# Performance work log

Hardware: AMD Instinct MI355X
Metric: run time of the kernel (lower is better)

## Reference

```python
import jax, jax.numpy as jnp
import numpy as np


def setup_inputs() -> dict:
    key = jax.random.key(0)
    ks = jax.random.split(key, 8)
    B, M, C, H, W = 2, 16, 256, 64, 64
    T = 1024  # transformer_dim
    return {
        "transformer_output": jax.random.normal(ks[0], (B, T), dtype=jnp.float32),
        "residual_maps": jax.random.normal(ks[1], (B, M, C, H, W), dtype=jnp.float32),
        "Wq": jax.random.normal(ks[2], (C, T), dtype=jnp.float32) * 0.02,
        "bq": jnp.zeros((C,), dtype=jnp.float32),
        "Wk": jax.random.normal(ks[3], (C, C), dtype=jnp.float32) * 0.02,
        "bk": jnp.zeros((C,), dtype=jnp.float32),
        "Wv": jax.random.normal(ks[4], (C, C), dtype=jnp.float32) * 0.02,
        "bv": jnp.zeros((C,), dtype=jnp.float32),
    }


def reference(transformer_output, residual_maps, Wq, bq, Wk, bk, Wv, bv):
    # residual_maps: [B, M, C, H, W]; single query per batch element.
    B, M, C, H, W = residual_maps.shape
    scale = C ** (-0.5)
    # Linear query projection: [B, C]
    q = transformer_output @ Wq.T + bq
    # 1x1 conv == per-pixel channel matmul: [B, M, C, H, W]
    keys = jnp.einsum("oc,bmchw->bmohw", Wk, residual_maps) + bk[None, None, :, None, None]
    values = jnp.einsum("oc,bmchw->bmohw", Wv, residual_maps) + bv[None, None, :, None, None]
    # Single-query dot-product scores per (map, pixel): [B, M, H, W]
    scores = jnp.einsum("bc,bmchw->bmhw", q, keys) * scale
    # Temporal softmax over num_maps at each spatial position
    probs = jax.nn.softmax(scores, axis=1)
    # Softmax-weighted sum of value maps: [B, C, H, W]
    out = jnp.einsum("bmhw,bmchw->bchw", probs, values)
    return out
```

## Files before the change

kernel.cpp:

```cpp
#include <hip/hip_runtime.h>

#define SCALE 0.0625f
#define ROW 36

typedef __attribute__((ext_vector_type(4))) float f32x4;
typedef __attribute__((ext_vector_type(8))) short s16x8;

__device__ __forceinline__ unsigned short f2bf(float x) {
    unsigned u = __float_as_uint(x);
    u = u + 0x7FFF + ((u >> 16) & 1);
    return (unsigned short)(u >> 16);
}

__global__ __launch_bounds__(256) void prep1_kernel(
    const float* __restrict__ TO,
    const float* __restrict__ Wq,
    const float* __restrict__ bq,
    const float* __restrict__ Wv,
    float* __restrict__ qbuf,
    unsigned short* __restrict__ WvB)
{
    const int blk = blockIdx.x;
    const int t   = threadIdx.x;
    if (blk < 16) {
        const int b    = blk >> 3;
        const int rblk = blk & 7;
        const int wv = t >> 6, l = t & 63;
        const float4* Wq4 = (const float4*)Wq;
        const float4* TO4 = (const float4*)TO;
        for (int rr = 0; rr < 8; ++rr) {
            const int c = rblk * 32 + wv * 8 + rr;
            float acc = 0.f;
#pragma unroll
            for (int i = 0; i < 4; ++i) {
                float4 wq = Wq4[c * 256 + i * 64 + l];
                float4 tv = TO4[b * 256 + i * 64 + l];
                acc = fmaf(wq.x, tv.x, acc);
                acc = fmaf(wq.y, tv.y, acc);
                acc = fmaf(wq.z, tv.z, acc);
                acc = fmaf(wq.w, tv.w, acc);
            }
#pragma unroll
            for (int mask = 1; mask < 64; mask <<= 1)
                acc += __shfl_xor(acc, mask, 64);
            if (l == 0) qbuf[b * 256 + c] = acc + bq[c];
        }
    } else {
        const int idx = blk - 16;
#pragma unroll
        for (int i = 0; i < 4; ++i) {
            const int e = idx * 4096 + i * 1024 + t * 4;
            const float4 f = ((const float4*)Wv)[e >> 2];
            ushort4 o;
            o.x = f2bf(f.x); o.y = f2bf(f.y);
            o.z = f2bf(f.z); o.w = f2bf(f.w);
            *(ushort4*)(WvB + e) = o;
        }
    }
}

__global__ __launch_bounds__(256) void prep2_kernel(
    const float* __restrict__ qbuf,
    const float* __restrict__ Wk,
    float* __restrict__ qks)
{
    const int blk = blockIdx.x;
    const int t   = threadIdx.x;
    const int b = blk >> 3, j = blk & 7;
    const int col = t & 31, chunk = t >> 5;
    const int cp = j * 32 + col;
    float partial = 0.f;
#pragma unroll 8
    for (int cc = 0; cc < 32; ++cc) {
        const int c = chunk * 32 + cc;
        partial = fmaf(qbuf[b * 256 + c], Wk[c * 256 + cp], partial);
    }
    __shared__ float r2[8][32];
    r2[chunk][col] = partial;
    __syncthreads();
    if (t < 32) {
        float s = 0.f;
#pragma unroll
        for (int k = 0; k < 8; ++k) s += r2[k][t];
        qks[b * 256 + j * 32 + t] = SCALE * s;
    }
}

__global__ __launch_bounds__(512, 2) void main_kernel(
    const float* __restrict__ X,
    const float* __restrict__ qks,
    const unsigned short* __restrict__ WvB,
    const float* __restrict__ bv,
    float* __restrict__ out)
{
    const int t    = threadIdx.x;
    const int lane = t & 63;
    const int w    = t >> 6;
    const int blk  = blockIdx.x;
    const int b    = blk >> 7;
    const int hw0  = (blk & 127) << 5;

    __shared__ float lds[2 * 256 * ROW];
    float* const buf0 = lds;
    float* const buf1 = lds + 256 * ROW;

    const int sc   = t >> 3;
    const int spxq = t & 7;
    const float4* X4 = (const float4*)X;
    const int gstage = b * 16 * 262144 + (hw0 >> 2) + spxq;

    float qk[4];
#pragma unroll
    for (int c4 = 0; c4 < 4; ++c4)
        qk[c4] = qks[b * 256 + lane + 64 * c4];

    float4 wx[4];
#pragma unroll
    for (int c4 = 0; c4 < 4; ++c4) wx[c4] = make_float4(0.f, 0.f, 0.f, 0.f);
    float lsx = 0.f, lsy = 0.f, lsz = 0.f, lsw = 0.f;

    float4 sreg[4];
#pragma unroll
    for (int r = 0; r < 4; ++r)
        sreg[r] = X4[gstage + 0 * 262144 + (sc + r * 64) * 1024];
#pragma unroll
    for (int r = 0; r < 4; ++r)
        *(float4*)&buf0[(sc + r * 64) * ROW + spxq * 4] = sreg[r];

#pragma unroll 2
    for (int m = 0; m < 16; ++m) {
        __syncthreads();
        float* const cur  = (m & 1) ? buf1 : buf0;
        float* const nxtb = (m & 1) ? buf0 : buf1;

        if (m < 15) {
#pragma unroll
            for (int r = 0; r < 4; ++r)
                sreg[r] = X4[gstage + (m + 1) * 262144 + (sc + r * 64) * 1024];
        }

        float4 v[4];
#pragma unroll
        for (int c4 = 0; c4 < 4; ++c4)
            v[c4] = *(const float4*)&cur[(lane + 64 * c4) * ROW + w * 4];

        float sx = 0.f, sy = 0.f, sz = 0.f, sw = 0.f;
#pragma unroll
        for (int c4 = 0; c4 < 4; ++c4) {
            sx = fmaf(qk[c4], v[c4].x, sx);
            sy = fmaf(qk[c4], v[c4].y, sy);
            sz = fmaf(qk[c4], v[c4].z, sz);
            sw = fmaf(qk[c4], v[c4].w, sw);
        }
#pragma unroll
        for (int mask = 1; mask < 64; mask <<= 1) {
            sx += __shfl_xor(sx, mask, 64);
            sy += __shfl_xor(sy, mask, 64);
            sz += __shfl_xor(sz, mask, 64);
            sw += __shfl_xor(sw, mask, 64);
        }
        const float e0 = __expf(sx), e1 = __expf(sy);
        const float e2 = __expf(sz), e3 = __expf(sw);
        lsx += e0; lsy += e1; lsz += e2; lsw += e3;
#pragma unroll
        for (int c4 = 0; c4 < 4; ++c4) {
            wx[c4].x = fmaf(e0, v[c4].x, wx[c4].x);
            wx[c4].y = fmaf(e1, v[c4].y, wx[c4].y);
            wx[c4].z = fmaf(e2, v[c4].z, wx[c4].z);
            wx[c4].w = fmaf(e3, v[c4].w, wx[c4].w);
        }

        if (m < 15) {
#pragma unroll
            for (int r = 0; r < 4; ++r)
                *(float4*)&nxtb[(sc + r * 64) * ROW + spxq * 4] = sreg[r];
        }
    }

    const float i0 = 1.0f / lsx, i1 = 1.0f / lsy;
    const float i2 = 1.0f / lsz, i3 = 1.0f / lsw;
#pragma unroll
    for (int c4 = 0; c4 < 4; ++c4) {
        float4 r;
        r.x = wx[c4].x * i0; r.y = wx[c4].y * i1;
        r.z = wx[c4].z * i2; r.w = wx[c4].w * i3;
        *(float4*)&buf0[(lane + 64 * c4) * ROW + w * 4] = r;
    }
    __syncthreads();

    const int px16 = lane & 15;
    const int quad = lane >> 4;

    f32x4 acc[2][2];
#pragma unroll
    for (int tl = 0; tl < 2; ++tl)
#pragma unroll
        for (int pxh = 0; pxh < 2; ++pxh)
#pragma unroll
            for (int r = 0; r < 4; ++r)
                acc[tl][pxh][r] = bv[16 * (w * 2 + tl) + quad * 4 + r];

#pragma unroll
    for (int ks = 0; ks < 8; ++ks) {
        s16x8 bfr[2];
#pragma unroll
        for (int pxh = 0; pxh < 2; ++pxh)
#pragma unroll
            for (int j = 0; j < 8; ++j)
                bfr[pxh][j] = (short)f2bf(
                    buf0[(ks * 32 + quad * 8 + j) * ROW + pxh * 16 + px16]);
#pragma unroll
        for (int tl = 0; tl < 2; ++tl) {
            const s16x8 afr = *(const s16x8*)(
                WvB + (16 * (w * 2 + tl) + px16) * 256 + ks * 32 + quad * 8);
#pragma unroll
            for (int pxh = 0; pxh < 2; ++pxh)
                acc[tl][pxh] = __builtin_amdgcn_mfma_f32_16x16x32_bf16(
                    afr, bfr[pxh], acc[tl][pxh], 0, 0, 0);
        }
    }

    const int obase = b * 256 * 4096 + hw0;
#pragma unroll
    for (int tl = 0; tl < 2; ++tl)
#pragma unroll
        for (int pxh = 0; pxh < 2; ++pxh)
#pragma unroll
            for (int r = 0; r < 4; ++r) {
                const int co = 16 * (w * 2 + tl) + quad * 4 + r;
                out[obase + co * 4096 + pxh * 16 + px16] = acc[tl][pxh][r];
            }
}

extern "C" void kernel_launch(void* const* d_in, const int* in_sizes, int n_in,
                              void* d_out, int out_size, void* d_ws, size_t ws_size,
                              hipStream_t stream) {
    const float* TO = (const float*)d_in[0];
    const float* X  = (const float*)d_in[1];
    const float* Wq = (const float*)d_in[2];
    const float* bq = (const float*)d_in[3];
    const float* Wk = (const float*)d_in[4];
    const float* Wv = (const float*)d_in[6];
    const float* bv = (const float*)d_in[7];
    float* out = (float*)d_out;
    float* ws  = (float*)d_ws;

    float*          qbuf = ws;
    float*          qks  = ws + 512;
    unsigned short* WvB  = (unsigned short*)(ws + 1024);

    hipLaunchKernelGGL(prep1_kernel, dim3(32), dim3(256), 0, stream,
                       TO, Wq, bq, Wv, qbuf, WvB);
    hipLaunchKernelGGL(prep2_kernel, dim3(16), dim3(256), 0, stream,
                       qbuf, Wk, qks);
    hipLaunchKernelGGL(main_kernel, dim3(256), dim3(512), 0, stream,
                       X, qks, WvB, bv, out);
}
```

Baseline: 234.7 us.

## Split fused attention kernel into score, softmax, weighted-sum and conv passes

Replaces the single fused main kernel, which streamed X through LDS with double buffering, with four kernels. A channel-chunked score pass writes partial scores, a softmax kernel reduces them, a weighted-sum pass re-reads X to form a bf16 intermediate, and a conv kernel applies the Wv MFMA. The aim is more parallelism and simpler, coalesced access in place of the LDS-bound fused loop. The cost is reading X twice (about 128 MB in total), extra global intermediates and extra launches, so the change is likely to be bandwidth-bound and slower.

```diff
diff --git a/kernel.cpp b/kernel.cpp
--- a/kernel.cpp
+++ b/kernel.cpp
@@ -5,6 +5,7 @@
 
 typedef __attribute__((ext_vector_type(4))) float f32x4;
 typedef __attribute__((ext_vector_type(8))) short s16x8;
+typedef __attribute__((ext_vector_type(8))) unsigned short u16x8;
 
 __device__ __forceinline__ unsigned short f2bf(float x) {
     unsigned u = __float_as_uint(x);
@@ -86,105 +87,127 @@
     }
 }
 
-__global__ __launch_bounds__(512, 2) void main_kernel(
+__global__ __launch_bounds__(512) void score_kernel(
     const float* __restrict__ X,
     const float* __restrict__ qks,
+    float* __restrict__ Sp)
+{
+    const int blk = blockIdx.x;
+    const int ch  = blk & 7;
+    const int bm  = blk >> 3;
+    const int b   = bm >> 4;
+    const int t   = threadIdx.x;
+    const int c0  = ch * 32;
+    const float4* X4 = (const float4*)X;
+    const int base = (bm * 256 + c0) * 1024;
+
+    float4 a0 = make_float4(0.f, 0.f, 0.f, 0.f);
+    float4 a1 = make_float4(0.f, 0.f, 0.f, 0.f);
+#pragma unroll 4
+    for (int c = 0; c < 32; ++c) {
+        const float q = qks[b * 256 + c0 + c];
+        const float4 x0 = X4[base + c * 1024 + t];
+        const float4 x1 = X4[base + c * 1024 + t + 512];
+        a0.x = fmaf(q, x0.x, a0.x); a0.y = fmaf(q, x0.y, a0.y);
+        a0.z = fmaf(q, x0.z, a0.z); a0.w = fmaf(q, x0.w, a0.w);
+        a1.x = fmaf(q, x1.x, a1.x); a1.y = fmaf(q, x1.y, a1.y);
+        a1.z = fmaf(q, x1.z, a1.z); a1.w = fmaf(q, x1.w, a1.w);
+    }
+    float4* S4 = (float4*)(Sp + (ch * 32 + bm) * 4096);
+    S4[t]       = a0;
+    S4[t + 512] = a1;
+}
+
+__global__ __launch_bounds__(128) void softmax_kernel(
+    const float* __restrict__ Sp,
+    float* __restrict__ P)
+{
+    const int blk = blockIdx.x;
+    const int b   = blk >> 5;
+    const int px  = ((blk & 31) << 7) + threadIdx.x;
+    float e[16];
+    float sum = 0.f;
+#pragma unroll
+    for (int m = 0; m < 16; ++m) {
+        float s = 0.f;
+#pragma unroll
+        for (int ch = 0; ch < 8; ++ch)
+            s += Sp[((ch * 2 + b) * 16 + m) * 4096 + px];
+        e[m] = __expf(s);
+        sum += e[m];
+    }
+    const float inv = 1.0f / sum;
+#pragma unroll
+    for (int m = 0; m < 16; ++m)
+        P[(b * 16 + m) * 4096 + px] = e[m] * inv;
+}
+
+__global__ __launch_bounds__(512) void wsum_kernel(
+    const float* __restrict__ X,
+    const float* __restrict__ P,
+    unsigned short* __restrict__ Ybf)
+{
+    const int blk = blockIdx.x;
+    const int ph  = blk & 1;
+    const int oc  = (blk >> 1) & 63;
+    const int b   = blk >> 7;
+    const int t   = threadIdx.x;
+    const int o0  = oc * 4;
+    const int px4 = (ph << 9) + t;
+    const float4* X4 = (const float4*)X;
+    const float4* P4 = (const float4*)P;
+
+    float4 acc[4];
+#pragma unroll
+    for (int o = 0; o < 4; ++o) acc[o] = make_float4(0.f, 0.f, 0.f, 0.f);
+
+#pragma unroll 2
+    for (int m = 0; m < 16; ++m) {
+        const float4 p = P4[(b * 16 + m) * 1024 + px4];
+#pragma unroll
+        for (int o = 0; o < 4; ++o) {
+            const float4 x = X4[((b * 16 + m) * 256 + o0 + o) * 1024 + px4];
+            acc[o].x = fmaf(p.x, x.x, acc[o].x);
+            acc[o].y = fmaf(p.y, x.y, acc[o].y);
+            acc[o].z = fmaf(p.z, x.z, acc[o].z);
+            acc[o].w = fmaf(p.w, x.w, acc[o].w);
+        }
+    }
+#pragma unroll
+    for (int o = 0; o < 4; ++o) {
+        ushort4 y;
+        y.x = f2bf(acc[o].x); y.y = f2bf(acc[o].y);
+        y.z = f2bf(acc[o].z); y.w = f2bf(acc[o].w);
+        *(ushort4*)(Ybf + (b * 256 + o0 + o) * 4096 + px4 * 4) = y;
+    }
+}
+
+__global__ __launch_bounds__(512) void conv_kernel(
+    const unsigned short* __restrict__ Ybf,
     const unsigned short* __restrict__ WvB,
     const float* __restrict__ bv,
     float* __restrict__ out)
 {
-    const int t    = threadIdx.x;
+    const int blk = blockIdx.x;
+    const int b   = blk >> 7;
+    const int px0 = (blk & 127) << 5;
+    const int t   = threadIdx.x;
     const int lane = t & 63;
     const int w    = t >> 6;
-    const int blk  = blockIdx.x;
-    const int b    = blk >> 7;
-    const int hw0  = (blk & 127) << 5;
-
-    __shared__ float lds[2 * 256 * ROW];
-    float* const buf0 = lds;
-    float* const buf1 = lds + 256 * ROW;
-
-    const int sc   = t >> 3;
-    const int spxq = t & 7;
-    const float4* X4 = (const float4*)X;
-    const int gstage = b * 16 * 262144 + (hw0 >> 2) + spxq;
-
-    float qk[4];
-#pragma unroll
-    for (int c4 = 0; c4 < 4; ++c4)
-        qk[c4] = qks[b * 256 + lane + 64 * c4];
-
-    float4 wx[4];
-#pragma unroll
-    for (int c4 = 0; c4 < 4; ++c4) wx[c4] = make_float4(0.f, 0.f, 0.f, 0.f);
-    float lsx = 0.f, lsy = 0.f, lsz = 0.f, lsw = 0.f;
-
-    float4 sreg[4];
-#pragma unroll
-    for (int r = 0; r < 4; ++r)
-        sreg[r] = X4[gstage + 0 * 262144 + (sc + r * 64) * 1024];
-#pragma unroll
-    for (int r = 0; r < 4; ++r)
-        *(float4*)&buf0[(sc + r * 64) * ROW + spxq * 4] = sreg[r];
-
-#pragma unroll 2
-    for (int m = 0; m < 16; ++m) {
-        __syncthreads();
-        float* const cur  = (m & 1) ? buf1 : buf0;
-        float* const nxtb = (m & 1) ? buf0 : buf1;
-
-        if (m < 15) {
-#pragma unroll
-            for (int r = 0; r < 4; ++r)
-                sreg[r] = X4[gstage + (m + 1) * 262144 + (sc + r * 64) * 1024];
-        }
-
-        float4 v[4];
-#pragma unroll
-        for (int c4 = 0; c4 < 4; ++c4)
-            v[c4] = *(const float4*)&cur[(lane + 64 * c4) * ROW + w * 4];
-
-        float sx = 0.f, sy = 0.f, sz = 0.f, sw = 0.f;
-#pragma unroll
-        for (int c4 = 0; c4 < 4; ++c4) {
-            sx = fmaf(qk[c4], v[c4].x, sx);
-            sy = fmaf(qk[c4], v[c4].y, sy);
-            sz = fmaf(qk[c4], v[c4].z, sz);
-            sw = fmaf(qk[c4], v[c4].w, sw);
-        }
-#pragma unroll
-        for (int mask = 1; mask < 64; mask <<= 1) {
-            sx += __shfl_xor(sx, mask, 64);
-            sy += __shfl_xor(sy, mask, 64);
-            sz += __shfl_xor(sz, mask, 64);
-            sw += __shfl_xor(sw, mask, 64);
-        }
-        const float e0 = __expf(sx), e1 = __expf(sy);
-        const float e2 = __expf(sz), e3 = __expf(sw);
-        lsx += e0; lsy += e1; lsz += e2; lsw += e3;
-#pragma unroll
-        for (int c4 = 0; c4 < 4; ++c4) {
-            wx[c4].x = fmaf(e0, v[c4].x, wx[c4].x);
-            wx[c4].y = fmaf(e1, v[c4].y, wx[c4].y);
-            wx[c4].z = fmaf(e2, v[c4].z, wx[c4].z);
-            wx[c4].w = fmaf(e3, v[c4].w, wx[c4].w);
-        }
-
-        if (m < 15) {
-#pragma unroll
-            for (int r = 0; r < 4; ++r)
-                *(float4*)&nxtb[(sc + r * 64) * ROW + spxq * 4] = sreg[r];
-        }
-    }
-
-    const float i0 = 1.0f / lsx, i1 = 1.0f / lsy;
-    const float i2 = 1.0f / lsz, i3 = 1.0f / lsw;
-#pragma unroll
-    for (int c4 = 0; c4 < 4; ++c4) {
-        float4 r;
-        r.x = wx[c4].x * i0; r.y = wx[c4].y * i1;
-        r.z = wx[c4].z * i2; r.w = wx[c4].w * i3;
-        *(float4*)&buf0[(lane + 64 * c4) * ROW + w * 4] = r;
+
+    __shared__ float slab[256 * ROW];
+
+    {
+        const int o = t >> 2, q = t & 3;
+#pragma unroll
+        for (int h = 0; h < 2; ++h) {
+            const int oo = o + h * 128;
+            const u16x8 v = *(const u16x8*)(Ybf + (b * 256 + oo) * 4096 + px0 + q * 8);
+#pragma unroll
+            for (int j = 0; j < 8; ++j)
+                slab[oo * ROW + q * 8 + j] =
+                    __uint_as_float((unsigned)(unsigned short)v[j] << 16);
+        }
     }
     __syncthreads();
 
@@ -208,7 +231,7 @@
 #pragma unroll
             for (int j = 0; j < 8; ++j)
                 bfr[pxh][j] = (short)f2bf(
-                    buf0[(ks * 32 + quad * 8 + j) * ROW + pxh * 16 + px16]);
+                    slab[(ks * 32 + quad * 8 + j) * ROW + pxh * 16 + px16]);
 #pragma unroll
         for (int tl = 0; tl < 2; ++tl) {
             const s16x8 afr = *(const s16x8*)(
@@ -220,7 +243,7 @@
         }
     }
 
-    const int obase = b * 256 * 4096 + hw0;
+    const int obase = b * 256 * 4096 + px0;
 #pragma unroll
     for (int tl = 0; tl < 2; ++tl)
 #pragma unroll
@@ -248,11 +271,20 @@
     float*          qbuf = ws;
     float*          qks  = ws + 512;
     unsigned short* WvB  = (unsigned short*)(ws + 1024);
+    float*          Sp   = ws + 33792;
+    float*          P    = ws + 1082368;
+    unsigned short* Ybf  = (unsigned short*)(ws + 1213440);
 
     hipLaunchKernelGGL(prep1_kernel, dim3(32), dim3(256), 0, stream,
                        TO, Wq, bq, Wv, qbuf, WvB);
     hipLaunchKernelGGL(prep2_kernel, dim3(16), dim3(256), 0, stream,
                        qbuf, Wk, qks);
-    hipLaunchKernelGGL(main_kernel, dim3(256), dim3(512), 0, stream,
-                       X, qks, WvB, bv, out);
-}
+    hipLaunchKernelGGL(score_kernel, dim3(256), dim3(512), 0, stream,
+                       X, qks, Sp);
+    hipLaunchKernelGGL(softmax_kernel, dim3(64), dim3(128), 0, stream,
+                       Sp, P);
+    hipLaunchKernelGGL(wsum_kernel, dim3(256), dim3(512), 0, stream,
+                       X, P, Ybf);
+    hipLaunchKernelGGL(conv_kernel, dim3(256), dim3(512), 0, stream,
+                       Ybf, WvB, bv, out);
+}
```

Measured after the change: 248.9 us. 6.1% more time.
